# Optimization experiments

Hardware: AMD Instinct MI355X
Metric: run time of the kernel (lower is better)

The kernel has to match this reference:

```python
import jax, jax.numpy as jnp
import numpy as np

TEMPERATURE = 0.1
N = 8192
V = 2
D = 512

def setup_inputs() -> dict:
    key = jax.random.key(0)
    k1, k2, k3 = jax.random.split(key, 3)
    features = jax.random.normal(k1, (N, V, D), dtype=jnp.float32)
    features1 = jax.random.normal(k2, (N, V, D), dtype=jnp.float32)
    y = jax.random.randint(k3, (N,), 0, 10, dtype=jnp.int64)
    return {"features": features, "features1": features1, "y": y}

def reference(features, features1, y):
    # Take view 0; L2-normalize anchors only (features1 is NOT normalized in the original).
    anchor = features[:, 0, :]
    anchor = anchor / jnp.linalg.norm(anchor, axis=1, keepdims=True)
    f1 = features1[:, 0, :]
    # sim: [N, N]
    sim = jnp.einsum('nd,md->nm', anchor, f1)
    # Original builds logits = [diag_i | row_i without diag] / T and uses label 0.
    # That concat is a permutation of the full row, so
    # CE(row) = logsumexp(row / T) - diag / T, averaged over rows.
    logits = sim / TEMPERATURE
    pos = jnp.diagonal(logits)  # [N]
    loss = jnp.mean(jax.nn.logsumexp(logits, axis=1) - pos)
    return loss
```

## Files before the change

### kernel.cpp

```cpp
#include <hip/hip_runtime.h>
#include <hip/hip_bf16.h>

typedef __attribute__((ext_vector_type(4)))  float f32x4;
typedef __attribute__((ext_vector_type(8)))  int   i32x8;
typedef __attribute__((ext_vector_type(4)))  int   i32x4;

static constexpr int NROW = 8192;
static constexpr int DDIM = 512;
static constexpr float INV_T = 10.0f;
static constexpr float SHIFT = 70.0f;
static constexpr float E2_SC = 14.4269504089f;
static constexpr float E2_BI = -100.988652759f;
static constexpr unsigned SCALE1 = 0x7F7F7F7Fu;

__device__ __forceinline__ void gload_lds16(const void* gsrc, void* ldst) {
  __builtin_amdgcn_global_load_lds(
      (const __attribute__((address_space(1))) unsigned int*)gsrc,
      (__attribute__((address_space(3))) unsigned int*)ldst, 16, 0, 0);
}

__device__ __forceinline__ float fast_exp2(float x) {
#if __has_builtin(__builtin_amdgcn_exp2f)
  return __builtin_amdgcn_exp2f(x);
#else
  float r;
  asm("v_exp_f32 %0, %1" : "=v"(r) : "v"(x));
  return r;
#endif
}

__device__ __forceinline__ unsigned int pack_fp8x4(float x, float y, float z, float w) {
  unsigned int r = 0;
  r = __builtin_amdgcn_cvt_pk_fp8_f32(x, y, r, false);
  r = __builtin_amdgcn_cvt_pk_fp8_f32(z, w, r, true);
  return r;
}

__global__ void prep_kernel(const float* __restrict__ f0,
                            const float* __restrict__ f1,
                            unsigned int* __restrict__ A,
                            unsigned int* __restrict__ B,
                            float* __restrict__ wsS,
                            float* __restrict__ wsPosRow) {
  int gid  = blockIdx.x * blockDim.x + threadIdx.x;
  if (gid < NROW) wsS[gid] = 0.f;
  int wid  = gid >> 6;
  int lane = threadIdx.x & 63;
  const float4* s0 = (const float4*)(f0 + (size_t)wid * (2 * DDIM));
  const float4* s1 = (const float4*)(f1 + (size_t)wid * (2 * DDIM));
  float4 v0 = s0[lane], v1 = s0[lane + 64];
  float4 w0 = s1[lane], w1 = s1[lane + 64];
  float ss = v0.x * v0.x + v0.y * v0.y + v0.z * v0.z + v0.w * v0.w +
             v1.x * v1.x + v1.y * v1.y + v1.z * v1.z + v1.w * v1.w;
  float cc = v0.x * w0.x + v0.y * w0.y + v0.z * w0.z + v0.w * w0.w +
             v1.x * w1.x + v1.y * w1.y + v1.z * w1.z + v1.w * w1.w;
#pragma unroll
  for (int m = 1; m < 64; m <<= 1) {
    ss += __shfl_xor(ss, m);
    cc += __shfl_xor(cc, m);
  }
  float rn = rsqrtf(ss);
  if (lane == 0) wsPosRow[wid] = cc * rn * INV_T;
  A[wid * 128 + lane]      = pack_fp8x4(v0.x * rn, v0.y * rn, v0.z * rn, v0.w * rn);
  A[wid * 128 + 64 + lane] = pack_fp8x4(v1.x * rn, v1.y * rn, v1.z * rn, v1.w * rn);
  B[wid * 128 + lane]      = pack_fp8x4(w0.x, w0.y, w0.z, w0.w);
  B[wid * 128 + 64 + lane] = pack_fp8x4(w1.x, w1.y, w1.z, w1.w);
}

__global__ __launch_bounds__(512, 2) void sim_lse_kernel(
    const unsigned char* __restrict__ Ag,
    const unsigned char* __restrict__ Bg,
    float* __restrict__ wsS) {
  __shared__ __align__(16) char bufA[64 * 512];
  __shared__ __align__(16) char bufB[64 * 512];

  const int tid  = threadIdx.x;
  const int w    = tid >> 6;
  const int lane = tid & 63;
  const int lr   = lane & 15;
  const int kg   = lane >> 4;

  const int p  = blockIdx.x >> 3;
  const int cs = blockIdx.x & 7;
  const int r0 = p * 256 + w * 32;
  const int c0 = cs * 1024;

  const int h5      = lane >> 5;
  const int stg_off = ((lane & 31) << 4) ^ (((2 * w + h5) & 7) << 4);
  const int stg_row = h5;
  const int swz = (lr & 7) << 4;

  i32x8 a0[4], a1[4];
  {
    const char* ar0 = (const char*)Ag + (size_t)(r0 + lr) * DDIM + kg * 32;
    const char* ar1 = (const char*)Ag + (size_t)(r0 + 16 + lr) * DDIM + kg * 32;
#pragma unroll
    for (int ks = 0; ks < 4; ks++) {
      a0[ks] = *(const i32x8*)(ar0 + ks * 128);
      a1[ks] = *(const i32x8*)(ar1 + ks * 128);
    }
  }

  float sums0[4], sums1[4];
#pragma unroll
  for (int r = 0; r < 4; r++) { sums0[r] = 0.f; sums1[r] = 0.f; }

#define STAGE(BUF, T)                                                          \
  {                                                                            \
    const char* gb = (const char*)Bg + (size_t)(c0 + (T) * 64) * DDIM;         \
    _Pragma("unroll")                                                          \
    for (int it = 0; it < 4; it++) {                                           \
      int pr = it * 8 + w;                                                     \
      gload_lds16(gb + (size_t)(2 * pr + stg_row) * DDIM + stg_off,            \
                  (char*)(BUF) + pr * 1024);                                   \
    }                                                                          \
  }

#define MFMA_EPI(BUF)                                                          \
  {                                                                            \
    _Pragma("unroll")                                                          \
    for (int jb = 0; jb < 4; jb++) {                                           \
      const int cb = ((jb * 16 + lr) * 512 + kg * 32) ^ swz;                   \
      const char* p0  = (const char*)(BUF) + cb;                               \
      const char* p0x = (const char*)(BUF) + (cb ^ 16);                        \
      f32x4 acc0 = (f32x4){0.f, 0.f, 0.f, 0.f};                                \
      f32x4 acc1 = (f32x4){0.f, 0.f, 0.f, 0.f};                                \
      __builtin_amdgcn_s_setprio(1);                                           \
      _Pragma("unroll")                                                        \
      for (int ks = 0; ks < 4; ks++) {                                         \
        i32x8 bv = __builtin_shufflevector(                                    \
            *(const i32x4*)(p0 + ks * 128), *(const i32x4*)(p0x + ks * 128),   \
            0, 1, 2, 3, 4, 5, 6, 7);                                           \
        acc0 = __builtin_amdgcn_mfma_scale_f32_16x16x128_f8f6f4(               \
            a0[ks], bv, acc0, 0, 0, 0, SCALE1, 0, SCALE1);                     \
        acc1 = __builtin_amdgcn_mfma_scale_f32_16x16x128_f8f6f4(               \
            a1[ks], bv, acc1, 0, 0, 0, SCALE1, 0, SCALE1);                     \
      }                                                                        \
      __builtin_amdgcn_s_setprio(0);                                           \
      _Pragma("unroll")                                                        \
      for (int r = 0; r < 4; r++) {                                            \
        sums0[r] += fast_exp2(fmaf(acc0[r], E2_SC, E2_BI));                    \
        sums1[r] += fast_exp2(fmaf(acc1[r], E2_SC, E2_BI));                    \
      }                                                                        \
    }                                                                          \
  }

  STAGE(bufA, 0);
  __syncthreads();

#pragma unroll 1
  for (int t = 0; t < 16; t += 2) {
    STAGE(bufB, t + 1);
    MFMA_EPI(bufA);
    __syncthreads();
    if (t + 2 < 16) STAGE(bufA, t + 2);
    MFMA_EPI(bufB);
    __syncthreads();
  }

#undef STAGE
#undef MFMA_EPI

#pragma unroll
  for (int r = 0; r < 4; r++) {
    float s0 = sums0[r], s1 = sums1[r];
    s0 += __shfl_xor(s0, 1);  s1 += __shfl_xor(s1, 1);
    s0 += __shfl_xor(s0, 2);  s1 += __shfl_xor(s1, 2);
    s0 += __shfl_xor(s0, 4);  s1 += __shfl_xor(s1, 4);
    s0 += __shfl_xor(s0, 8);  s1 += __shfl_xor(s1, 8);
    if (lr == 0) {
      atomicAdd(&wsS[r0 + kg * 4 + r], s0);
      atomicAdd(&wsS[r0 + 16 + kg * 4 + r], s1);
    }
  }
}

__global__ void finalize_kernel(const float* __restrict__ wsS,
                                const float* __restrict__ wsPosRow,
                                float* __restrict__ out) {
  __shared__ float red[16];
  float part = 0.f;
  for (int r = threadIdx.x; r < NROW; r += 1024)
    part += SHIFT + __logf(wsS[r]) - wsPosRow[r];
#pragma unroll
  for (int m = 1; m < 64; m <<= 1) part += __shfl_xor(part, m);
  if ((threadIdx.x & 63) == 0) red[threadIdx.x >> 6] = part;
  __syncthreads();
  if (threadIdx.x < 16) {
    float t = red[threadIdx.x];
#pragma unroll
    for (int m = 1; m < 16; m <<= 1) t += __shfl_xor(t, m);
    if (threadIdx.x == 0) out[0] = t / (float)NROW;
  }
}

extern "C" void kernel_launch(void* const* d_in, const int* in_sizes, int n_in,
                              void* d_out, int out_size, void* d_ws, size_t ws_size,
                              hipStream_t stream) {
  const float* f0 = (const float*)d_in[0];
  const float* f1 = (const float*)d_in[1];

  unsigned char* A = (unsigned char*)d_ws;
  unsigned char* B = A + (size_t)NROW * DDIM;
  float* wsS      = (float*)(B + (size_t)NROW * DDIM);
  float* wsPosRow = wsS + NROW;

  prep_kernel<<<NROW / 4, 256, 0, stream>>>(f0, f1, (unsigned int*)A,
                                            (unsigned int*)B, wsS, wsPosRow);
  sim_lse_kernel<<<256, 512, 0, stream>>>(A, B, wsS);
  finalize_kernel<<<1, 1024, 0, stream>>>(wsS, wsPosRow, (float*)d_out);
}
```

Measured before the change: 54.95 us.

## Triple-buffer B tiles with partial vmcnt waits to overlap loads with MFMA

Replaces the double-buffered LDS staging of B tiles with a three-buffer rotation. Each step issues the next tile's async global-to-LDS load after computing, then waits only until the older tile has landed (vmcnt(4)) before the barrier. The intent is to keep two tiles of loads in flight so global latency hides behind MFMA work and full drains at every sync are avoided. LDS use grows to 96KB per block, which may limit the two-blocks-per-CU target. Correctness also depends on the exact count of outstanding vector memory operations.

```diff
diff --git a/kernel.cpp b/kernel.cpp
--- a/kernel.cpp
+++ b/kernel.cpp
@@ -71,8 +71,9 @@
     const unsigned char* __restrict__ Ag,
     const unsigned char* __restrict__ Bg,
     float* __restrict__ wsS) {
-  __shared__ __align__(16) char bufA[64 * 512];
-  __shared__ __align__(16) char bufB[64 * 512];
+  __shared__ __align__(16) char buf0[64 * 512];
+  __shared__ __align__(16) char buf1[64 * 512];
+  __shared__ __align__(16) char buf2[64 * 512];
 
   const int tid  = threadIdx.x;
   const int w    = tid >> 6;
@@ -145,21 +146,37 @@
     }                                                                          \
   }
 
-  STAGE(bufA, 0);
-  __syncthreads();
+#define WAITBAR4()                                                             \
+  {                                                                            \
+    asm volatile("s_waitcnt vmcnt(4)" ::: "memory");                           \
+    __builtin_amdgcn_s_barrier();                                              \
+  }
+#define WAITBAR0()                                                             \
+  {                                                                            \
+    asm volatile("s_waitcnt vmcnt(0)" ::: "memory");                           \
+    __builtin_amdgcn_s_barrier();                                              \
+  }
+
+  STAGE(buf0, 0);
+  STAGE(buf1, 1);
+  WAITBAR4();
 
 #pragma unroll 1
-  for (int t = 0; t < 16; t += 2) {
-    STAGE(bufB, t + 1);
-    MFMA_EPI(bufA);
-    __syncthreads();
-    if (t + 2 < 16) STAGE(bufA, t + 2);
-    MFMA_EPI(bufB);
-    __syncthreads();
-  }
+  for (int i = 0; i < 4; i++) {
+    const int t = 3 * i;
+    MFMA_EPI(buf0);  STAGE(buf2, t + 2);  WAITBAR4();
+    MFMA_EPI(buf1);  STAGE(buf0, t + 3);  WAITBAR4();
+    MFMA_EPI(buf2);  STAGE(buf1, t + 4);  WAITBAR4();
+  }
+  MFMA_EPI(buf0);  STAGE(buf2, 14);  WAITBAR4();
+  MFMA_EPI(buf1);  STAGE(buf0, 15);  WAITBAR4();
+  MFMA_EPI(buf2);  WAITBAR0();
+  MFMA_EPI(buf0);
 
 #undef STAGE
 #undef MFMA_EPI
+#undef WAITBAR4
+#undef WAITBAR0
 
 #pragma unroll
   for (int r = 0; r < 4; r++) {
```

New measurement: 48.49 us, median of 2. 11.8% less time.

## Deepen LDS pipeline to four buffers and fuse finalize via last-block reduction

Applied to the files above, without the earlier changes.

Replaces the two-buffer staging with a four-buffer ring that keeps three tile loads in flight, synchronising with explicit vmcnt waits and barriers instead of full syncthreads. The separate finalize kernel is removed: the last block to finish, detected with an atomic counter zeroed in prep, computes the final loss. This aims to hide more global-load latency and save a kernel launch. In exchange it doubles shared memory per block, which lowers possible occupancy, and it adds a fence and atomic at the end of the kernel.

```diff
diff --git a/kernel.cpp b/kernel.cpp
--- a/kernel.cpp
+++ b/kernel.cpp
@@ -41,9 +41,11 @@
                             unsigned int* __restrict__ A,
                             unsigned int* __restrict__ B,
                             float* __restrict__ wsS,
-                            float* __restrict__ wsPosRow) {
+                            float* __restrict__ wsPosRow,
+                            int* __restrict__ wsCnt) {
   int gid  = blockIdx.x * blockDim.x + threadIdx.x;
   if (gid < NROW) wsS[gid] = 0.f;
+  if (gid == 0) *wsCnt = 0;
   int wid  = gid >> 6;
   int lane = threadIdx.x & 63;
   const float4* s0 = (const float4*)(f0 + (size_t)wid * (2 * DDIM));
@@ -70,9 +72,14 @@
 __global__ __launch_bounds__(512, 2) void sim_lse_kernel(
     const unsigned char* __restrict__ Ag,
     const unsigned char* __restrict__ Bg,
-    float* __restrict__ wsS) {
-  __shared__ __align__(16) char bufA[64 * 512];
-  __shared__ __align__(16) char bufB[64 * 512];
+    float* __restrict__ wsS,
+    const float* __restrict__ wsPosRow,
+    int* __restrict__ wsCnt,
+    float* __restrict__ out) {
+  __shared__ __align__(16) char buf0[64 * 512];
+  __shared__ __align__(16) char buf1[64 * 512];
+  __shared__ __align__(16) char buf2[64 * 512];
+  __shared__ __align__(16) char buf3[64 * 512];
 
   const int tid  = threadIdx.x;
   const int w    = tid >> 6;
@@ -145,21 +152,33 @@
     }                                                                          \
   }
 
-  STAGE(bufA, 0);
-  __syncthreads();
+#define WAITBAR(N)                                                             \
+  {                                                                            \
+    asm volatile("s_waitcnt vmcnt(" #N ")" ::: "memory");                      \
+    __builtin_amdgcn_s_barrier();                                              \
+  }
+
+  STAGE(buf0, 0);
+  STAGE(buf1, 1);
+  STAGE(buf2, 2);
+  WAITBAR(8);
 
 #pragma unroll 1
-  for (int t = 0; t < 16; t += 2) {
-    STAGE(bufB, t + 1);
-    MFMA_EPI(bufA);
-    __syncthreads();
-    if (t + 2 < 16) STAGE(bufA, t + 2);
-    MFMA_EPI(bufB);
-    __syncthreads();
-  }
+  for (int i = 0; i < 3; i++) {
+    const int t = 4 * i;
+    MFMA_EPI(buf0);  STAGE(buf3, t + 3);  WAITBAR(8);
+    MFMA_EPI(buf1);  STAGE(buf0, t + 4);  WAITBAR(8);
+    MFMA_EPI(buf2);  STAGE(buf1, t + 5);  WAITBAR(8);
+    MFMA_EPI(buf3);  STAGE(buf2, t + 6);  WAITBAR(8);
+  }
+  MFMA_EPI(buf0);  STAGE(buf3, 15);  WAITBAR(8);
+  MFMA_EPI(buf1);  WAITBAR(4);
+  MFMA_EPI(buf2);  WAITBAR(0);
+  MFMA_EPI(buf3);
 
 #undef STAGE
 #undef MFMA_EPI
+#undef WAITBAR
 
 #pragma unroll
   for (int r = 0; r < 4; r++) {
@@ -173,24 +192,28 @@
       atomicAdd(&wsS[r0 + 16 + kg * 4 + r], s1);
     }
   }
-}
-
-__global__ void finalize_kernel(const float* __restrict__ wsS,
-                                const float* __restrict__ wsPosRow,
-                                float* __restrict__ out) {
-  __shared__ float red[16];
-  float part = 0.f;
-  for (int r = threadIdx.x; r < NROW; r += 1024)
-    part += SHIFT + __logf(wsS[r]) - wsPosRow[r];
-#pragma unroll
-  for (int m = 1; m < 64; m <<= 1) part += __shfl_xor(part, m);
-  if ((threadIdx.x & 63) == 0) red[threadIdx.x >> 6] = part;
+
+  __threadfence();
   __syncthreads();
-  if (threadIdx.x < 16) {
-    float t = red[threadIdx.x];
-#pragma unroll
-    for (int m = 1; m < 16; m <<= 1) t += __shfl_xor(t, m);
-    if (threadIdx.x == 0) out[0] = t / (float)NROW;
+  int* flag = (int*)buf0;
+  if (tid == 0) flag[0] = (atomicAdd(wsCnt, 1) == 255) ? 1 : 0;
+  __syncthreads();
+  if (flag[0]) {
+    float part = 0.f;
+    for (int r = tid; r < NROW; r += 512)
+      part += SHIFT + __logf(atomicAdd(&wsS[r], 0.f)) - wsPosRow[r];
+#pragma unroll
+    for (int m = 1; m < 64; m <<= 1) part += __shfl_xor(part, m);
+    float* red = (float*)(buf0 + 256);
+    if (lane == 0) red[w] = part;
+    __syncthreads();
+    if (tid < 8) {
+      float t = red[tid];
+      t += __shfl_xor(t, 1);
+      t += __shfl_xor(t, 2);
+      t += __shfl_xor(t, 4);
+      if (tid == 0) out[0] = t / (float)NROW;
+    }
   }
 }
 
@@ -204,9 +227,11 @@
   unsigned char* B = A + (size_t)NROW * DDIM;
   float* wsS      = (float*)(B + (size_t)NROW * DDIM);
   float* wsPosRow = wsS + NROW;
+  int*   wsCnt    = (int*)(wsPosRow + NROW);
 
   prep_kernel<<<NROW / 4, 256, 0, stream>>>(f0, f1, (unsigned int*)A,
-                                            (unsigned int*)B, wsS, wsPosRow);
-  sim_lse_kernel<<<256, 512, 0, stream>>>(A, B, wsS);
-  finalize_kernel<<<1, 1024, 0, stream>>>(wsS, wsPosRow, (float*)d_out);
-}
+                                            (unsigned int*)B, wsS, wsPosRow,
+                                            wsCnt);
+  sim_lse_kernel<<<256, 512, 0, stream>>>(A, B, wsS, wsPosRow, wsCnt,
+                                          (float*)d_out);
+}
```

Measured after the change: 80.92 us. +47.3%, slower.
